# Kernel tuning notes

Hardware: AMD Instinct MI355X
Metric: run time of the kernel (lower is better)

The kernel has to match this reference:

```python
import jax, jax.numpy as jnp
import numpy as np

DIM, D_STATE, D_CONV, EXPAND = 512, 16, 4, 2
D_INNER = EXPAND * DIM            # 1024
DT_RANK = (DIM + 15) // 16        # 32
B, L = 2, 2048


def setup_inputs() -> dict:
    key = jax.random.key(0)
    ks = jax.random.split(key, 12)
    s_in = 1.0 / np.sqrt(DIM)
    s_xp = 1.0 / np.sqrt(D_INNER)
    s_dt = 1.0 / np.sqrt(DT_RANK)
    return {
        "x": jax.random.normal(ks[0], (B, L, DIM), jnp.float32),
        "ln_g": jnp.ones((DIM,), jnp.float32),
        "ln_b": jnp.zeros((DIM,), jnp.float32),
        "W_in": jax.random.normal(ks[1], (2 * D_INNER, DIM), jnp.float32) * s_in,
        "conv_w": jax.random.normal(ks[2], (D_INNER, D_CONV), jnp.float32) * 0.5,
        "conv_b": jax.random.normal(ks[3], (D_INNER,), jnp.float32) * 0.1,
        "W_xproj": jax.random.normal(ks[4], (DT_RANK + 2 * D_STATE, D_INNER), jnp.float32) * s_xp,
        "W_dt": jax.random.normal(ks[5], (D_INNER, DT_RANK), jnp.float32) * s_dt,
        "b_dt": jax.random.normal(ks[6], (D_INNER,), jnp.float32) * 0.1 - 4.0,  # softplus -> small dt
        "A_log": jnp.log(jax.random.uniform(ks[7], (D_INNER, D_STATE), jnp.float32, 1.0, 16.0)),
        "Dp": jax.random.normal(ks[8], (D_INNER,), jnp.float32),
        "W_out": jax.random.normal(ks[9], (DIM, D_INNER), jnp.float32) * s_xp,
    }


def _layernorm(x, g, b, eps=1e-5):
    mu = jnp.mean(x, -1, keepdims=True)
    var = jnp.mean(jnp.square(x - mu), -1, keepdims=True)
    return (x - mu) * jax.lax.rsqrt(var + eps) * g + b


def reference(x, ln_g, ln_b, W_in, conv_w, conv_b, W_xproj, W_dt, b_dt, A_log, Dp, W_out):
    h = _layernorm(x, ln_g, ln_b)
    # input projection -> [B,L,2*d_inner]
    xz = jnp.einsum('bld,ed->ble', h, W_in)
    xp, z = jnp.split(xz, 2, axis=-1)
    # depthwise causal conv1d over time (kernel d_conv), then SiLU
    xp_pad = jnp.pad(xp, ((0, 0), (D_CONV - 1, 0), (0, 0)))
    xc = conv_b
    for k in range(D_CONV):
        xc = xc + xp_pad[:, k:k + L, :] * conv_w[:, k]
    xc = jax.nn.silu(xc)
    # x_proj -> dt, B, C
    proj = jnp.einsum('bld,ed->ble', xc, W_xproj)
    dt_r = proj[..., :DT_RANK]
    Bm = proj[..., DT_RANK:DT_RANK + D_STATE]          # [B,L,n]
    Cm = proj[..., DT_RANK + D_STATE:]                 # [B,L,n]
    dt = jax.nn.softplus(jnp.einsum('blr,dr->bld', dt_r, W_dt) + b_dt)  # [B,L,d]
    A = -jnp.exp(A_log)                                # [d,n]
    dA = jnp.exp(jnp.einsum('bld,dn->bldn', dt, A))    # [B,L,d,n]
    dBx = dt[..., None] * Bm[:, :, None, :] * xc[..., None]  # [B,L,d,n]
    # selective scan over time (time-major for lax.scan)
    def step(s, inp):
        dA_t, dBx_t, C_t = inp
        s = s * dA_t + dBx_t                           # [B,d,n]
        y_t = jnp.einsum('bdn,bn->bd', s, C_t)
        return s, y_t
    s0 = jnp.zeros((B, D_INNER, D_STATE), xc.dtype)
    _, ys = jax.lax.scan(step, s0,
                         (jnp.moveaxis(dA, 1, 0), jnp.moveaxis(dBx, 1, 0), jnp.moveaxis(Cm, 1, 0)))
    y = jnp.moveaxis(ys, 0, 1)                         # [B,L,d]
    y = y + xc * Dp
    y = y * jax.nn.silu(z)
    out = jnp.einsum('bld,ed->ble', y, W_out)
    return x + out  # dropout is identity in eval mode
```

## Files before the change

kernel.cpp:

```cpp
#include <hip/hip_runtime.h>
#include <hip/hip_bf16.h>
#include <math.h>

#define B_      2
#define L_      2048
#define DIM_    512
#define DINNER  1024
#define DTRANK  32
#define DSTATE  16
#define DCONV   4
#define BL      (B_ * L_)
#define NCHUNK  64
#define CLEN    (L_ / NCHUNK)

typedef __attribute__((ext_vector_type(8))) short bf16x8;
typedef __attribute__((ext_vector_type(4))) float f32x4;

static __device__ __forceinline__ unsigned short f2bf(float f) {
  __hip_bfloat16 h = __float2bfloat16(f);
  return *(unsigned short*)&h;
}
static __device__ __forceinline__ float bf2f(unsigned short u) {
  return __uint_as_float(((unsigned int)u) << 16);
}

static __device__ __forceinline__ void gload16(const void* g, void* l) {
  __builtin_amdgcn_global_load_lds(
      (const __attribute__((address_space(1))) void*)g,
      (__attribute__((address_space(3))) void*)l, 16, 0, 0);
}

static __device__ __forceinline__ float softplus_f(float acc) {
  return (acc > 20.f) ? acc : __logf(1.f + __expf(acc));
}

__global__ __launch_bounds__(256) void cvt_ln_kernel(
    const float* __restrict__ s0, const float* __restrict__ s1,
    const float* __restrict__ s2, __hip_bfloat16* __restrict__ d0,
    __hip_bfloat16* __restrict__ d1, __hip_bfloat16* __restrict__ d2,
    const float* __restrict__ x, const float* __restrict__ g,
    const float* __restrict__ b, __hip_bfloat16* __restrict__ h) {
  int blk = blockIdx.x;
  if (blk < 1600) {
    int i = (blk * 256 + threadIdx.x) * 4;
    const float* s; __hip_bfloat16* d; int off;
    if (i < 1048576)            { s = s0; d = d0; off = i; }
    else if (i < 1048576+65536) { s = s1; d = d1; off = i - 1048576; }
    else                        { s = s2; d = d2; off = i - 1114112; }
    float4 v = *(const float4*)(s + off);
    d[off + 0] = __float2bfloat16(v.x);
    d[off + 1] = __float2bfloat16(v.y);
    d[off + 2] = __float2bfloat16(v.z);
    d[off + 3] = __float2bfloat16(v.w);
    return;
  }
  int row = (blk - 1600) * 4 + (threadIdx.x >> 6);
  int lane = threadIdx.x & 63;
  const float* xr = x + (size_t)row * DIM_;
  float v[8];
  float sum = 0.f;
#pragma unroll
  for (int i = 0; i < 8; i++) { v[i] = xr[lane + i * 64]; sum += v[i]; }
#pragma unroll
  for (int o = 32; o > 0; o >>= 1) sum += __shfl_xor(sum, o, 64);
  float mu = sum * (1.f / DIM_);
  float vs = 0.f;
#pragma unroll
  for (int i = 0; i < 8; i++) { float dd = v[i] - mu; vs += dd * dd; }
#pragma unroll
  for (int o = 32; o > 0; o >>= 1) vs += __shfl_xor(vs, o, 64);
  float rstd = rsqrtf(vs * (1.f / DIM_) + 1e-5f);
  __hip_bfloat16* hr = h + (size_t)row * DIM_;
#pragma unroll
  for (int i = 0; i < 8; i++) {
    int c = lane + i * 64;
    hr[c] = __float2bfloat16((v[i] - mu) * rstd * g[c] + b[c]);
  }
}

template <bool ADD_RES, bool OUT_BF16>
__global__ __launch_bounds__(256) void gemm_mfma_128(
    const __hip_bfloat16* __restrict__ A, int lda,
    const __hip_bfloat16* __restrict__ Bw, int ldb,
    const float* __restrict__ Res, int ldr,
    void* __restrict__ C, int ldc, int K) {
  __shared__ short As[128 * 64];
  __shared__ short Bs[128 * 64];
  int t = threadIdx.x;
  int n0 = blockIdx.x * 128, m0 = blockIdx.y * 128;
  int w = t >> 6, lane = t & 63;
  int wm = (w >> 1) * 64, wn = (w & 1) * 64;
  int l15 = lane & 15, quad = lane >> 4;
  int lr = lane >> 3, lc = (lane & 7) * 8;
  const short* Ag = (const short*)A + (size_t)(m0 + w * 32 + lr) * lda + lc;
  const short* Bg = (const short*)Bw + (size_t)(n0 + w * 32 + lr) * ldb + lc;
  f32x4 acc[4][4];
#pragma unroll
  for (int i = 0; i < 4; i++)
#pragma unroll
    for (int j = 0; j < 4; j++) acc[i][j] = (f32x4){0.f, 0.f, 0.f, 0.f};
  for (int k0 = 0; k0 < K; k0 += 64) {
    __syncthreads();
#pragma unroll
    for (int p = 0; p < 4; p++) {
      gload16(Ag + (size_t)(p * 8) * lda + k0, &As[(w * 32 + p * 8) * 64]);
      gload16(Bg + (size_t)(p * 8) * ldb + k0, &Bs[(w * 32 + p * 8) * 64]);
    }
    __syncthreads();
#pragma unroll
    for (int kk = 0; kk < 64; kk += 32) {
      bf16x8 af[4], bfr[4];
#pragma unroll
      for (int i = 0; i < 4; i++) {
        af[i] = *(const bf16x8*)&As[(wm + i * 16 + l15) * 64 + kk + quad * 8];
        bfr[i] = *(const bf16x8*)&Bs[(wn + i * 16 + l15) * 64 + kk + quad * 8];
      }
#pragma unroll
      for (int i = 0; i < 4; i++)
#pragma unroll
        for (int j = 0; j < 4; j++)
          acc[i][j] = __builtin_amdgcn_mfma_f32_16x16x32_bf16(
              af[i], bfr[j], acc[i][j], 0, 0, 0);
    }
  }
#pragma unroll
  for (int i = 0; i < 4; i++)
#pragma unroll
    for (int r = 0; r < 4; r++) {
      int row = m0 + wm + i * 16 + quad * 4 + r;
#pragma unroll
      for (int j = 0; j < 4; j++) {
        int col = n0 + wn + j * 16 + l15;
        float v = acc[i][j][r];
        if (ADD_RES) v += Res[(size_t)row * ldr + col];
        if (OUT_BF16)
          ((unsigned short*)C)[(size_t)row * ldc + col] = f2bf(v);
        else
          ((float*)C)[(size_t)row * ldc + col] = v;
      }
    }
}

template <bool ADD_RES>
__global__ __launch_bounds__(256) void gemm_mfma_64(
    const __hip_bfloat16* __restrict__ A, int lda,
    const __hip_bfloat16* __restrict__ Bw, int ldb,
    const float* __restrict__ Res, int ldr,
    float* __restrict__ C, int ldc, int K, size_t czs) {
  __shared__ short As[64 * 64];
  __shared__ short Bs[64 * 64];
  int t = threadIdx.x;
  int n0 = blockIdx.x * 64, m0 = blockIdx.y * 64;
  size_t kbase = (size_t)blockIdx.z * K;
  int w = t >> 6, lane = t & 63;
  int wm = (w >> 1) * 32, wn = (w & 1) * 32;
  int l15 = lane & 15, quad = lane >> 4;
  int lr = lane >> 3, lc = (lane & 7) * 8;
  const short* Ag = (const short*)A + (size_t)(m0 + w * 16 + lr) * lda + lc + kbase;
  const short* Bg = (const short*)Bw + (size_t)(n0 + w * 16 + lr) * ldb + lc + kbase;
  f32x4 acc[2][2];
#pragma unroll
  for (int i = 0; i < 2; i++)
#pragma unroll
    for (int j = 0; j < 2; j++) acc[i][j] = (f32x4){0.f, 0.f, 0.f, 0.f};
  for (int k0 = 0; k0 < K; k0 += 64) {
    __syncthreads();
#pragma unroll
    for (int p = 0; p < 2; p++) {
      gload16(Ag + (size_t)(p * 8) * lda + k0, &As[(w * 16 + p * 8) * 64]);
      gload16(Bg + (size_t)(p * 8) * ldb + k0, &Bs[(w * 16 + p * 8) * 64]);
    }
    __syncthreads();
#pragma unroll
    for (int kk = 0; kk < 64; kk += 32) {
      bf16x8 af[2], bfr[2];
#pragma unroll
      for (int i = 0; i < 2; i++) {
        af[i] = *(const bf16x8*)&As[(wm + i * 16 + l15) * 64 + kk + quad * 8];
        bfr[i] = *(const bf16x8*)&Bs[(wn + i * 16 + l15) * 64 + kk + quad * 8];
      }
#pragma unroll
      for (int i = 0; i < 2; i++)
#pragma unroll
        for (int j = 0; j < 2; j++)
          acc[i][j] = __builtin_amdgcn_mfma_f32_16x16x32_bf16(
              af[i], bfr[j], acc[i][j], 0, 0, 0);
    }
  }
  float* Cz = C + czs * blockIdx.z;
#pragma unroll
  for (int i = 0; i < 2; i++)
#pragma unroll
    for (int r = 0; r < 4; r++) {
      int row = m0 + wm + i * 16 + quad * 4 + r;
#pragma unroll
      for (int j = 0; j < 2; j++) {
        int col = n0 + wn + j * 16 + l15;
        float v = acc[i][j][r];
        if (ADD_RES) v += Res[(size_t)row * ldr + col];
        Cz[(size_t)row * ldc + col] = v;
      }
    }
}

__global__ __launch_bounds__(256) void gemm_proj_conv(
    const unsigned short* __restrict__ xzb,
    const __hip_bfloat16* __restrict__ Bw,
    const float* __restrict__ cw, const float* __restrict__ cb,
    __hip_bfloat16* __restrict__ xc_bf,
    float* __restrict__ C, size_t czs) {
  __shared__ short As[64 * 64];
  __shared__ short Bs[64 * 64];
  __shared__ float cws[256 * 4];
  __shared__ float cbs[256];
  int t = threadIdx.x;
  int m0 = blockIdx.y * 64;
  int kbase = blockIdx.z * 256;
  int w = t >> 6, lane = t & 63;
  int wm = (w >> 1) * 32, wn = (w & 1) * 32;
  int l15 = lane & 15, quad = lane >> 4;
  int lrB = lane >> 3, lcB = (lane & 7) * 8;
  const short* Bg = (const short*)Bw + (size_t)(w * 16 + lrB) * DINNER + lcB + kbase;
  *(float4*)&cws[t * 4] = *(const float4*)(cw + (size_t)(kbase + t) * 4);
  cbs[t] = cb[kbase + t];
  int ar = t >> 2, aq = t & 3;
  int bl = m0 + ar;
  int l = bl & (L_ - 1);
  f32x4 acc[2][2];
#pragma unroll
  for (int i = 0; i < 2; i++)
#pragma unroll
    for (int j = 0; j < 2; j++) acc[i][j] = (f32x4){0.f, 0.f, 0.f, 0.f};
  for (int k0 = 0; k0 < 256; k0 += 64) {
    __syncthreads();
#pragma unroll
    for (int p = 0; p < 2; p++)
      gload16(Bg + k0 + (size_t)(p * 8) * DINNER, &Bs[(w * 16 + p * 8) * 64]);
    int dl0 = k0 + aq * 16;
    const unsigned short* xrow = xzb + (size_t)bl * 2048 + kbase + dl0;
    float o[16];
#pragma unroll
    for (int cc = 0; cc < 16; cc++) o[cc] = cbs[dl0 + cc];
#pragma unroll
    for (int k = 0; k < 4; k++) {
      int off = 3 - k;
      bool ok = (l >= off);
      const unsigned short* src = xrow - (size_t)(ok ? off : 0) * 2048;
      bf16x8 v0 = *(const bf16x8*)(src);
      bf16x8 v1 = *(const bf16x8*)(src + 8);
#pragma unroll
      for (int cc = 0; cc < 8; cc++) {
        float xa = ok ? bf2f((unsigned short)v0[cc]) : 0.f;
        float xb = ok ? bf2f((unsigned short)v1[cc]) : 0.f;
        o[cc]     = fmaf(xa, cws[(dl0 + cc) * 4 + k], o[cc]);
        o[cc + 8] = fmaf(xb, cws[(dl0 + cc + 8) * 4 + k], o[cc + 8]);
      }
    }
    bf16x8 pa, pb;
#pragma unroll
    for (int cc = 0; cc < 8; cc++) {
      float va = o[cc] / (1.f + __expf(-o[cc]));
      float vb = o[cc + 8] / (1.f + __expf(-o[cc + 8]));
      pa[cc] = (short)f2bf(va);
      pb[cc] = (short)f2bf(vb);
    }
    *(bf16x8*)&As[ar * 64 + aq * 16] = pa;
    *(bf16x8*)&As[ar * 64 + aq * 16 + 8] = pb;
    unsigned short* xcd = (unsigned short*)xc_bf + (size_t)bl * DINNER + kbase + dl0;
    *(bf16x8*)xcd = pa;
    *(bf16x8*)(xcd + 8) = pb;
    __syncthreads();
#pragma unroll
    for (int kk = 0; kk < 64; kk += 32) {
      bf16x8 af[2], bfr[2];
#pragma unroll
      for (int i = 0; i < 2; i++) {
        af[i] = *(const bf16x8*)&As[(wm + i * 16 + l15) * 64 + kk + quad * 8];
        bfr[i] = *(const bf16x8*)&Bs[(wn + i * 16 + l15) * 64 + kk + quad * 8];
      }
#pragma unroll
      for (int i = 0; i < 2; i++)
#pragma unroll
        for (int j = 0; j < 2; j++)
          acc[i][j] = __builtin_amdgcn_mfma_f32_16x16x32_bf16(
              af[i], bfr[j], acc[i][j], 0, 0, 0);
    }
  }
  float* Cz = C + czs * blockIdx.z;
#pragma unroll
  for (int i = 0; i < 2; i++)
#pragma unroll
    for (int r = 0; r < 4; r++) {
      int row = m0 + wm + i * 16 + quad * 4 + r;
#pragma unroll
      for (int j = 0; j < 2; j++) {
        int col = wn + j * 16 + l15;
        Cz[(size_t)row * 64 + col] = acc[i][j][r];
      }
    }
}

__global__ __launch_bounds__(256) void dt_kernel(
    const float* __restrict__ pp, float* __restrict__ proj,
    const float* __restrict__ Wdt, const float* __restrict__ bdt,
    float* __restrict__ dt) {
  int blk = blockIdx.x;
  int dgrp = blk & 3;
  int bl0 = (blk >> 2) * 8;
  int tid = threadIdx.x;
  int d = dgrp * 256 + tid;
  __shared__ float pr[8 * 64];
  float w[32];
#pragma unroll
  for (int q = 0; q < 8; q++) {
    float4 wv = *(const float4*)(Wdt + (size_t)d * 32 + q * 4);
    w[q * 4 + 0] = wv.x; w[q * 4 + 1] = wv.y;
    w[q * 4 + 2] = wv.z; w[q * 4 + 3] = wv.w;
  }
  float bias = bdt[d];
  if (tid < 128) {
    int o4 = bl0 * 16 + tid;
    float4 v0 = ((const float4*)pp)[o4];
    float4 v1 = ((const float4*)pp)[o4 + 65536];
    float4 v2 = ((const float4*)pp)[o4 + 131072];
    float4 v3 = ((const float4*)pp)[o4 + 196608];
    float4 s;
    s.x = (v0.x + v1.x) + (v2.x + v3.x);
    s.y = (v0.y + v1.y) + (v2.y + v3.y);
    s.z = (v0.z + v1.z) + (v2.z + v3.z);
    s.w = (v0.w + v1.w) + (v2.w + v3.w);
    ((float4*)pr)[tid] = s;
    if (dgrp == 0) *(float4*)(proj + (size_t)bl0 * 64 + tid * 4) = s;
  }
  __syncthreads();
#pragma unroll
  for (int row = 0; row < 8; row++) {
    float a0 = 0.f, a1 = 0.f, a2 = 0.f, a3 = 0.f;
#pragma unroll
    for (int q = 0; q < 8; q++) {
      float4 pv = *(const float4*)&pr[row * 64 + q * 4];
      a0 = fmaf(pv.x, w[q * 4 + 0], a0);
      a1 = fmaf(pv.y, w[q * 4 + 1], a1);
      a2 = fmaf(pv.z, w[q * 4 + 2], a2);
      a3 = fmaf(pv.w, w[q * 4 + 3], a3);
    }
    float acc = bias + ((a0 + a1) + (a2 + a3));
    dt[(size_t)(bl0 + row) * DINNER + d] = softplus_f(acc);
  }
}

__global__ __launch_bounds__(256) void scan1_kernel(
    const float* __restrict__ dt, const __hip_bfloat16* __restrict__ xc_bf,
    const float* __restrict__ proj, const float* __restrict__ A_log,
    float* __restrict__ T, float* __restrict__ E) {
  int bid = blockIdx.x;
  int dgrp = bid & 63;
  int c = (bid >> 6) & (NCHUNK - 1);
  int b = bid >> 12;
  int tid = threadIdx.x;
  int n = tid & 15;
  int dl = tid >> 4;
  int d = dgrp * 16 + dl;
  int l0 = c * CLEN;
  __shared__ float dts[CLEN * 16];
  __shared__ float dxs[CLEN * 16];
  __shared__ float Bsh[CLEN * 16];
  for (int i = tid; i < CLEN * 16; i += 256) {
    int row = i >> 4, col = i & 15;
    size_t bl = (size_t)(b * L_ + l0 + row);
    float dtv = dt[bl * DINNER + dgrp * 16 + col];
    float xv = __bfloat162float(xc_bf[bl * DINNER + dgrp * 16 + col]);
    dts[i] = dtv;
    dxs[i] = dtv * xv;
    Bsh[i] = proj[bl * 64 + 32 + col];
  }
  float Aa = -__expf(A_log[(size_t)d * 16 + n]);
  __syncthreads();
  float Tn = 1.f, En = 0.f;
#pragma unroll 8
  for (int l = 0; l < CLEN; l++) {
    float dA = __expf(dts[l * 16 + dl] * Aa);
    Tn *= dA;
    En = En * dA + dxs[l * 16 + dl] * Bsh[l * 16 + n];
  }
  size_t o = (((size_t)b * NCHUNK + c) * DINNER + d) * 16 + n;
  T[o] = Tn; E[o] = En;
}

__global__ __launch_bounds__(256) void combine_kernel(
    float* __restrict__ T, const float* __restrict__ E) {
  int idx = blockIdx.x * 256 + threadIdx.x;
  int b = idx >> 14;
  int dn = idx & 16383;
  size_t base = (size_t)b * NCHUNK * (DINNER * 16) + dn;
  float s = 0.f;
#pragma unroll
  for (int batch = 0; batch < 4; batch++) {
    float t[16], e[16];
#pragma unroll
    for (int j = 0; j < 16; j++) {
      size_t o = base + (size_t)(batch * 16 + j) * (DINNER * 16);
      t[j] = T[o]; e[j] = E[o];
    }
#pragma unroll
    for (int j = 0; j < 16; j++) {
      T[base + (size_t)(batch * 16 + j) * (DINNER * 16)] = s;
      s = t[j] * s + e[j];
    }
  }
}

__global__ __launch_bounds__(256) void scan2_kernel(
    const float* __restrict__ dt, const __hip_bfloat16* __restrict__ xc_bf,
    const float* __restrict__ proj, const float* __restrict__ A_log,
    const float* __restrict__ Sstart, const float* __restrict__ Dp,
    unsigned short* __restrict__ xzb) {
  int bid = blockIdx.x;
  int dgrp = bid & 3;
  int c = (bid >> 2) & (NCHUNK - 1);
  int b = bid >> 8;
  int tid = threadIdx.x;
  int d = dgrp * 256 + tid;
  int l0 = c * CLEN;
  __shared__ float Bsh[CLEN * 16];
  __shared__ float Csh[CLEN * 16];
  for (int i = tid; i < CLEN * 16; i += 256) {
    int row = i >> 4, nn = i & 15;
    const float* pr = proj + (size_t)(b * L_ + l0 + row) * 64;
    Bsh[i] = pr[32 + nn];
    Csh[i] = pr[48 + nn];
  }
  float dtr[CLEN], xvr[CLEN];
  unsigned short zr[CLEN];
#pragma unroll
  for (int l = 0; l < CLEN; l++) {
    size_t bl = (size_t)(b * L_ + l0 + l);
    dtr[l] = dt[bl * DINNER + d];
    xvr[l] = __bfloat162float(xc_bf[bl * DINNER + d]);
    zr[l] = xzb[bl * 2048 + 1024 + d];
  }
  float Aa[16], s[16];
  size_t sb = (((size_t)b * NCHUNK + c) * DINNER + d) * 16;
#pragma unroll
  for (int q = 0; q < 4; q++) {
    float4 av = *(const float4*)(A_log + (size_t)d * 16 + q * 4);
    Aa[q * 4 + 0] = -__expf(av.x); Aa[q * 4 + 1] = -__expf(av.y);
    Aa[q * 4 + 2] = -__expf(av.z); Aa[q * 4 + 3] = -__expf(av.w);
    float4 sv = *(const float4*)(Sstart + sb + q * 4);
    s[q * 4 + 0] = sv.x; s[q * 4 + 1] = sv.y;
    s[q * 4 + 2] = sv.z; s[q * 4 + 3] = sv.w;
  }
  float Dv = Dp[d];
  __syncthreads();
#pragma unroll
  for (int l = 0; l < CLEN; l++) {
    float dtv = dtr[l];
    float xv = xvr[l];
    float dx = dtv * xv;
    float y = 0.f;
#pragma unroll
    for (int n = 0; n < 16; n++) {
      float dA = __expf(dtv * Aa[n]);
      s[n] = s[n] * dA + dx * Bsh[l * 16 + n];
      y += s[n] * Csh[l * 16 + n];
    }
    float zv = bf2f(zr[l]);
    float gate = zv / (1.f + __expf(-zv));
    xzb[(size_t)(b * L_ + l0 + l) * 2048 + d] = f2bf((y + xv * Dv) * gate);
  }
}

extern "C" void kernel_launch(void* const* d_in, const int* in_sizes, int n_in,
                              void* d_out, int out_size, void* d_ws, size_t ws_size,
                              hipStream_t stream) {
  const float* x      = (const float*)d_in[0];
  const float* ln_g   = (const float*)d_in[1];
  const float* ln_b   = (const float*)d_in[2];
  const float* W_in   = (const float*)d_in[3];
  const float* conv_w = (const float*)d_in[4];
  const float* conv_b = (const float*)d_in[5];
  const float* W_xprj = (const float*)d_in[6];
  const float* W_dt   = (const float*)d_in[7];
  const float* b_dt   = (const float*)d_in[8];
  const float* A_log  = (const float*)d_in[9];
  const float* Dp     = (const float*)d_in[10];
  const float* W_out  = (const float*)d_in[11];
  float* out = (float*)d_out;

  float* ws     = (float*)d_ws;
  float* xzb_f  = ws;
  float* xcbf_f = xzb_f + 4194304;
  float* proj   = xcbf_f + 2097152;
  float* pp     = proj + 262144;
  float* dtb    = pp + 1048576;
  float* T      = dtb + 4194304;
  float* E      = T + 2097152;
  float* hbf_f  = E + 2097152;
  float* wbf    = hbf_f + 1048576;

  unsigned short* xzb   = (unsigned short*)xzb_f;
  __hip_bfloat16* xc_bf = (__hip_bfloat16*)xcbf_f;
  __hip_bfloat16* h_bf  = (__hip_bfloat16*)hbf_f;
  __hip_bfloat16* Wb_in = (__hip_bfloat16*)wbf;
  __hip_bfloat16* Wb_xp = Wb_in + 1048576;
  __hip_bfloat16* Wb_out = Wb_xp + 65536;
  __hip_bfloat16* y_bf  = (__hip_bfloat16*)xzb;

  cvt_ln_kernel<<<1600 + BL / 4, 256, 0, stream>>>(
      W_in, W_xprj, W_out, Wb_in, Wb_xp, Wb_out, x, ln_g, ln_b, h_bf);
  gemm_mfma_128<false, true><<<dim3(2 * DINNER / 128, BL / 128), 256, 0, stream>>>(
      h_bf, DIM_, Wb_in, DIM_, nullptr, 0, xzb, 2 * DINNER, DIM_);
  gemm_proj_conv<<<dim3(1, BL / 64, 4), 256, 0, stream>>>(
      xzb, Wb_xp, conv_w, conv_b, xc_bf, pp, 262144);
  dt_kernel<<<(BL / 8) * 4, 256, 0, stream>>>(pp, proj, W_dt, b_dt, dtb);
  scan1_kernel<<<B_ * NCHUNK * 64, 256, 0, stream>>>(dtb, xc_bf, proj, A_log, T, E);
  combine_kernel<<<(B_ * DINNER * 16) / 256, 256, 0, stream>>>(T, E);
  scan2_kernel<<<B_ * NCHUNK * 4, 256, 0, stream>>>(dtb, xc_bf, proj, A_log, T, Dp, xzb);
  gemm_mfma_64<true><<<dim3(DIM_ / 64, BL / 64, 1), 256, 0, stream>>>(
      y_bf, 2048, Wb_out, DINNER, x, DIM_, out, DIM_, DINNER, 0);
}
```

Measured before the change: 190.9 us.

## Rework scan1 so each thread handles four states over 64 channels

The chunk-scan first pass now has each thread own four state entries of one channel, with a block covering 64 channels instead of 16. Loads of dt, xc and B into shared memory use float4 and bf16x8 vector accesses, and T/E are written as float4. This cuts the block count by four and shares each dt/xc shared-memory read across four states, which is meant to reduce load and launch overhead. In exchange each thread needs more registers and there are fewer blocks to fill the GPU.

```diff
diff --git a/kernel.cpp b/kernel.cpp
--- a/kernel.cpp
+++ b/kernel.cpp
@@ -354,37 +354,55 @@
     const float* __restrict__ proj, const float* __restrict__ A_log,
     float* __restrict__ T, float* __restrict__ E) {
   int bid = blockIdx.x;
-  int dgrp = bid & 63;
-  int c = (bid >> 6) & (NCHUNK - 1);
-  int b = bid >> 12;
+  int dgrp4 = bid & 15;
+  int c = (bid >> 4) & (NCHUNK - 1);
+  int b = bid >> 10;
   int tid = threadIdx.x;
-  int n = tid & 15;
-  int dl = tid >> 4;
-  int d = dgrp * 16 + dl;
+  int dl = tid >> 2;
+  int n4 = tid & 3;
+  int d0 = dgrp4 * 64;
+  int d = d0 + dl;
   int l0 = c * CLEN;
-  __shared__ float dts[CLEN * 16];
-  __shared__ float dxs[CLEN * 16];
+  __shared__ float dts[CLEN * 64];
+  __shared__ float xcs[CLEN * 64];
   __shared__ float Bsh[CLEN * 16];
   for (int i = tid; i < CLEN * 16; i += 256) {
-    int row = i >> 4, col = i & 15;
-    size_t bl = (size_t)(b * L_ + l0 + row);
-    float dtv = dt[bl * DINNER + dgrp * 16 + col];
-    float xv = __bfloat162float(xc_bf[bl * DINNER + dgrp * 16 + col]);
-    dts[i] = dtv;
-    dxs[i] = dtv * xv;
-    Bsh[i] = proj[bl * 64 + 32 + col];
-  }
-  float Aa = -__expf(A_log[(size_t)d * 16 + n]);
+    int row = i >> 4, c4 = i & 15;
+    *(float4*)&dts[row * 64 + c4 * 4] =
+        *(const float4*)(dt + (size_t)(b * L_ + l0 + row) * DINNER + d0 + c4 * 4);
+  }
+  {
+    int row = tid >> 3, c8 = tid & 7;
+    bf16x8 v = *(const bf16x8*)((const unsigned short*)xc_bf +
+                                (size_t)(b * L_ + l0 + row) * DINNER + d0 + c8 * 8);
+#pragma unroll
+    for (int k = 0; k < 8; k++)
+      xcs[row * 64 + c8 * 8 + k] = bf2f((unsigned short)v[k]);
+  }
+  if (tid < CLEN * 4) {
+    int row = tid >> 2, c4 = tid & 3;
+    *(float4*)&Bsh[row * 16 + c4 * 4] =
+        *(const float4*)(proj + (size_t)(b * L_ + l0 + row) * 64 + 32 + c4 * 4);
+  }
+  float4 av = *(const float4*)(A_log + (size_t)d * 16 + n4 * 4);
+  float Aa[4] = {-__expf(av.x), -__expf(av.y), -__expf(av.z), -__expf(av.w)};
   __syncthreads();
-  float Tn = 1.f, En = 0.f;
+  float Tn[4] = {1.f, 1.f, 1.f, 1.f};
+  float En[4] = {0.f, 0.f, 0.f, 0.f};
 #pragma unroll 8
   for (int l = 0; l < CLEN; l++) {
-    float dA = __expf(dts[l * 16 + dl] * Aa);
-    Tn *= dA;
-    En = En * dA + dxs[l * 16 + dl] * Bsh[l * 16 + n];
-  }
-  size_t o = (((size_t)b * NCHUNK + c) * DINNER + d) * 16 + n;
-  T[o] = Tn; E[o] = En;
+    float dtv = dts[l * 64 + dl];
+    float dx = dtv * xcs[l * 64 + dl];
+#pragma unroll
+    for (int j = 0; j < 4; j++) {
+      float dA = __expf(dtv * Aa[j]);
+      Tn[j] *= dA;
+      En[j] = En[j] * dA + dx * Bsh[l * 16 + n4 * 4 + j];
+    }
+  }
+  size_t o = (((size_t)b * NCHUNK + c) * DINNER + d) * 16 + n4 * 4;
+  *(float4*)&T[o] = *(float4*)Tn;
+  *(float4*)&E[o] = *(float4*)En;
 }
 
 __global__ __launch_bounds__(256) void combine_kernel(
@@ -513,7 +531,7 @@
   gemm_proj_conv<<<dim3(1, BL / 64, 4), 256, 0, stream>>>(
       xzb, Wb_xp, conv_w, conv_b, xc_bf, pp, 262144);
   dt_kernel<<<(BL / 8) * 4, 256, 0, stream>>>(pp, proj, W_dt, b_dt, dtb);
-  scan1_kernel<<<B_ * NCHUNK * 64, 256, 0, stream>>>(dtb, xc_bf, proj, A_log, T, E);
+  scan1_kernel<<<B_ * NCHUNK * 16, 256, 0, stream>>>(dtb, xc_bf, proj, A_log, T, E);
   combine_kernel<<<(B_ * DINNER * 16) / 256, 256, 0, stream>>>(T, E);
   scan2_kernel<<<B_ * NCHUNK * 4, 256, 0, stream>>>(dtb, xc_bf, proj, A_log, T, Dp, xzb);
   gemm_mfma_64<true><<<dim3(DIM_ / 64, BL / 64, 1), 256, 0, stream>>>(
```

New measurement: 191.9 us. No clear change (+0.5%).
